# Kernel optimization log

Measured on AMD Instinct MI355X. Metric: run time of the kernel, lower is better.

## Reference

```python
import jax, jax.numpy as jnp
import numpy as np

N, IN_DIM, D, H, E_DIM, G, NPG = 512, 16, 256, 8, 6, 32, 16
C = D           # per-head channels in GATv2Conv/TransformerConv (out_channels=d_model)
HD = D // H     # MultiheadAttention head dim


def _ln(x, g, b, eps=1e-5):
    m = jnp.mean(x, -1, keepdims=True)
    v = jnp.mean((x - m) ** 2, -1, keepdims=True)
    return (x - m) * jax.lax.rsqrt(v + eps) * g + b


def _seg_softmax(logits, seg, n):
    # numerically stable softmax over edges grouped by destination node
    m = jax.ops.segment_max(logits, seg, num_segments=n)
    m = jnp.where(jnp.isfinite(m), m, 0.0)
    e = jnp.exp(logits - m[seg])
    s = jax.ops.segment_sum(e, seg, num_segments=n)
    return e / jnp.maximum(s[seg], 1e-16)


def _forward(x, edge_attr, emb_w, emb_b, emb_g, emb_bb, pe, gat_lw, gat_lb, gat_rw, gat_rb, gat_ew, gat_att, gat_bias, tq_w, tq_b, tk_w, tk_b, tv_w, tv_b, te_w, tskip_w, tskip_b, tbeta_w, ln_g, ln_b, mha_in_w, mha_in_b, mha_out_w, mha_out_b, pool_w, pool_b, c1_w, c1_b, c1_g, c1_bb, rb_w, rb_b, rb_g, rb_bb, c2_w, c2_b, edge_index, batch):
    src, dst = edge_index[0], edge_index[1]
    E = edge_attr.shape[0]
    # input embedding (Linear + LayerNorm) + learned positional encoding (eval: no dropout)
    h = _ln(x @ emb_w.T + emb_b, emb_g, emb_bb) + pe[:N]
    residual = h
    # --- GATv2Conv(d_model, d_model, heads=H, edge_dim=6, concat=False, add_self_loops=False) ---
    xl = (h @ gat_lw.T + gat_lb).reshape(N, H, C)          # source transform
    xr = (h @ gat_rw.T + gat_rb).reshape(N, H, C)          # target transform
    ee = (edge_attr @ gat_ew.T).reshape(E, H, C)
    z = jax.nn.leaky_relu(xl[src] + xr[dst] + ee, 0.2)
    a = _seg_softmax(jnp.einsum('ehc,hc->eh', z, gat_att), dst, N)
    x_gat = jax.ops.segment_sum(xl[src] * a[..., None], dst, num_segments=N).mean(1) + gat_bias
    x_gat = _ln(x_gat, ln_g, ln_b)
    # --- TransformerConv(d_model, d_model, heads=H, edge_dim=6, concat=False, beta=True) ---
    te = (edge_attr @ te_w.T).reshape(E, H, C)
    q = (x_gat @ tq_w.T + tq_b).reshape(N, H, C)[dst]
    k = (x_gat @ tk_w.T + tk_b).reshape(N, H, C)[src] + te
    v = (x_gat @ tv_w.T + tv_b).reshape(N, H, C)[src] + te
    a2 = _seg_softmax((q * k).sum(-1) / np.sqrt(C).astype(np.float32), dst, N)
    out = jax.ops.segment_sum(v * a2[..., None], dst, num_segments=N).mean(1)
    r = x_gat @ tskip_w.T + tskip_b
    beta = jax.nn.sigmoid(jnp.concatenate([out, r, out - r], -1) @ tbeta_w.T)
    x_tr = _ln(beta * r + (1.0 - beta) * out, ln_g, ln_b)
    # --- dynamic attention mask: after the repeat/permute/reshape gymnastics this equals
    #     ds[:N] repeated H*N times, reshaped to [H, N, N] ---
    im = edge_attr[:, 5]
    ds = jnp.exp(-0.5 * ((im - 125.09) / 15.0) ** 2)
    ds = 1.0 - (ds - ds.min()) / (ds.max() - ds.min())
    mask = jnp.repeat(ds[:N], H * N).reshape(H, N, N)
    # --- cross MultiheadAttention (query=x_tr, key=x_gat, value=h, attn_mask added) ---
    wq, wk, wv = jnp.split(mha_in_w, 3, axis=0)
    bq, bk, bv = jnp.split(mha_in_b, 3, axis=0)
    qh = ((x_tr @ wq.T + bq) / np.sqrt(HD).astype(np.float32)).reshape(N, H, HD).transpose(1, 0, 2)
    kh = (x_gat @ wk.T + bk).reshape(N, H, HD).transpose(1, 0, 2)
    vh = (h @ wv.T + bv).reshape(N, H, HD).transpose(1, 0, 2)
    attn = jax.nn.softmax(qh @ kh.transpose(0, 2, 1) + mask, axis=-1)   # [H,N,N]
    o = (attn @ vh).transpose(1, 0, 2).reshape(N, D) @ mha_out_w.T + mha_out_b
    # torch broadcast of [N,1,D] attn output + [N,D] residual -> [N,N,D]
    x3 = o[:, None, :] + residual[None, :, :]
    # attention pooling: softmax over a size-1 dim yields all-ones scores (kept faithfully)
    x2 = x3.reshape(N * N, D)
    brep = jnp.tile(batch, N)
    score = jax.nn.softmax(x2 @ pool_w.T + pool_b, axis=1)
    pooled = jax.ops.segment_sum(score * x2, brep, num_segments=G)
    # classifier: Linear->LN->GELU->ResidualBlockv2->Linear (dropout off in eval)
    c = jax.nn.gelu(_ln(pooled @ c1_w.T + c1_b, c1_g, c1_bb), approximate=False)
    c = c + jax.nn.gelu(_ln(c @ rb_w.T + rb_b, rb_g, rb_bb), approximate=False)
    return c @ c2_w.T + c2_b   # [G, 1]


def setup_inputs():
    key = jax.random.key(0)
    ks = iter(jax.random.split(key, 64))
    f = lambda *sh: 0.02 * jax.random.normal(next(ks), sh, jnp.float32)
    # G fully-connected directed cliques of NPG nodes (no self loops) -> every node has in-edges
    i = np.arange(NPG)
    s, t = np.meshgrid(i, i, indexing='ij')
    msk = s != t
    s, t = s[msk], t[msk]
    off = (np.arange(G) * NPG)[:, None]
    edge_index = jnp.asarray(np.stack([(s[None] + off).reshape(-1), (t[None] + off).reshape(-1)]), jnp.int32)
    E = edge_index.shape[1]
    batch = jnp.asarray(np.repeat(np.arange(G), NPG), jnp.int32)
    x = jax.random.normal(next(ks), (N, IN_DIM), jnp.float32)
    edge_attr = jax.random.normal(next(ks), (E, E_DIM), jnp.float32)
    edge_attr = edge_attr.at[:, 5].set(edge_attr[:, 5] * 30.0 + 125.0)  # invariant-mass-like column
    HC = H * C
    return dict(
        x=x, edge_attr=edge_attr,
        emb_w=f(D, IN_DIM), emb_b=f(D), emb_g=jnp.ones(D), emb_bb=jnp.zeros(D),
        pe=f(1000, D),
        gat_lw=f(HC, D), gat_lb=f(HC), gat_rw=f(HC, D), gat_rb=f(HC),
        gat_ew=f(HC, E_DIM), gat_att=f(H, C), gat_bias=f(C),
        tq_w=f(HC, D), tq_b=f(HC), tk_w=f(HC, D), tk_b=f(HC),
        tv_w=f(HC, D), tv_b=f(HC), te_w=f(HC, E_DIM),
        tskip_w=f(D, D), tskip_b=f(D), tbeta_w=f(1, 3 * D),
        ln_g=jnp.ones(D), ln_b=jnp.zeros(D),
        mha_in_w=f(3 * D, D), mha_in_b=f(3 * D), mha_out_w=f(D, D), mha_out_b=f(D),
        pool_w=f(1, D), pool_b=f(1),
        c1_w=f(128, D), c1_b=f(128), c1_g=jnp.ones(128), c1_bb=jnp.zeros(128),
        rb_w=f(128, 128), rb_b=f(128), rb_g=jnp.ones(128), rb_bb=jnp.zeros(128),
        c2_w=f(1, 128), c2_b=f(1),
        edge_index=edge_index, batch=batch)


def reference(x, edge_attr, emb_w, emb_b, emb_g, emb_bb, pe, gat_lw, gat_lb, gat_rw, gat_rb, gat_ew, gat_att, gat_bias, tq_w, tq_b, tk_w, tk_b, tv_w, tv_b, te_w, tskip_w, tskip_b, tbeta_w, ln_g, ln_b, mha_in_w, mha_in_b, mha_out_w, mha_out_b, pool_w, pool_b, c1_w, c1_b, c1_g, c1_bb, rb_w, rb_b, rb_g, rb_bb, c2_w, c2_b, edge_index, batch):
    return _forward(x, edge_attr, emb_w, emb_b, emb_g, emb_bb, pe, gat_lw, gat_lb, gat_rw, gat_rb, gat_ew, gat_att, gat_bias, tq_w, tq_b, tk_w, tk_b, tv_w, tv_b, te_w, tskip_w, tskip_b, tbeta_w, ln_g, ln_b, mha_in_w, mha_in_b, mha_out_w, mha_out_b, pool_w, pool_b, c1_w, c1_b, c1_g, c1_bb, rb_w, rb_b, rb_g, rb_bb, c2_w, c2_b, edge_index, batch)
```

## Files before the change

kernel.cpp:

```cpp
#include <hip/hip_runtime.h>
#include <hip/hip_bf16.h>
#include <math.h>

#define NN 512
#define DM 256
#define NH 8
#define NG 32
#define NPG 16
#define INDIM 16
#define BIGW (2048 * 256)

typedef __hip_bfloat16 bf16;
typedef __attribute__((ext_vector_type(8))) short short8;
typedef __attribute__((ext_vector_type(4))) float f32x4;

__device__ __forceinline__ float b2f(bf16 v) { return __bfloat162float(v); }
__device__ __forceinline__ bf16 f2b(float v) { return __float2bfloat16(v); }
__device__ __forceinline__ short f2bs(float v) { bf16 t = __float2bfloat16(v); return *(short*)&t; }
__device__ __forceinline__ float fin(float v) {
    return (v == v && v > -1e30f && v < 1e30f) ? v : 0.f;
}
__device__ __forceinline__ int is_bf16(const void* ones_arr) {
    return ((const unsigned short*)ones_arr)[0] == 0x3F80u;
}

__device__ __forceinline__ void unpack8(uint4 u, float* w) {
    unsigned uu[4] = {u.x, u.y, u.z, u.w};
    #pragma unroll
    for (int j = 0; j < 4; j++) {
        __hip_bfloat162 b2 = *reinterpret_cast<const __hip_bfloat162*>(&uu[j]);
        float2 f = __bfloat1622float2(b2);
        w[2 * j] = f.x; w[2 * j + 1] = f.y;
    }
}
__device__ __forceinline__ float4 bload4(const bf16* p) {
    uint2 u = *(const uint2*)p;
    __hip_bfloat162 a = *reinterpret_cast<const __hip_bfloat162*>(&u.x);
    __hip_bfloat162 b = *reinterpret_cast<const __hip_bfloat162*>(&u.y);
    float2 f0 = __bfloat1622float2(a), f1 = __bfloat1622float2(b);
    return make_float4(f0.x, f0.y, f1.x, f1.y);
}

__device__ __forceinline__ float dot256(const float* xrow, const bf16* wrow) {
    const uint4* w4 = (const uint4*)wrow;
    uint4 q = w4[0];
    float acc = 0.f;
    for (int k8 = 0; k8 < 32; k8++) {
        uint4 qn = w4[(k8 + 1) & 31];
        float w[8]; unpack8(q, w);
        const float4* sp = (const float4*)&xrow[k8 * 8];
        float4 a0 = sp[0], a1 = sp[1];
        acc += a0.x*w[0] + a0.y*w[1] + a0.z*w[2] + a0.w*w[3]
             + a1.x*w[4] + a1.y*w[5] + a1.z*w[6] + a1.w*w[7];
        q = qn;
    }
    return acc;
}

template<int BS>
__device__ __forceinline__ float ln_norm(float v, float g, float b, float* red) {
    int t = threadIdx.x;
    red[t] = v; __syncthreads();
    for (int s = BS / 2; s > 0; s >>= 1) { if (t < s) red[t] += red[t + s]; __syncthreads(); }
    float mean = red[0] * (1.0f / (float)BS); __syncthreads();
    float d = v - mean;
    red[t] = d * d; __syncthreads();
    for (int s = BS / 2; s > 0; s >>= 1) { if (t < s) red[t] += red[t + s]; __syncthreads(); }
    float var = red[0] * (1.0f / (float)BS); __syncthreads();
    return d * rsqrtf(var + 1e-5f) * g + b;
}

struct CvtTab { const void* p[35]; int cum[36]; };
struct Cvt5 { const void* p[5]; };
__global__ void k_convert_all(Cvt5 tab5, CvtTab tab, const void* ones, bf16* wbig,
                              bf16* wbuf, float* gz, int nz) {
    int i = blockIdx.x * 256 + threadIdx.x;
    int a = blockIdx.y;
    int bf = is_bf16(ones);
    if (a < 5) {
        if (i >= BIGW) return;
        float v = bf ? b2f(((const bf16*)tab5.p[a])[i]) : ((const float*)tab5.p[a])[i];
        int row = i >> 8, k = i & 255;
        int hh = row >> 8, col = row & 255;
        int T = col >> 4, n16 = col & 15;
        int ks = k >> 5, quad = (k >> 3) & 3, j = k & 7;
        int dst = ((((hh * 16 + T) * 8 + ks) * 4 + quad) * 16 + n16) * 8 + j;
        wbig[(size_t)a * BIGW + dst] = f2b(v);
    } else {
        if (i < tab.cum[35]) {
            int aa = 0;
            while (i >= tab.cum[aa + 1]) aa++;
            int off = i - tab.cum[aa];
            float v = bf ? b2f(((const bf16*)tab.p[aa])[off]) : ((const float*)tab.p[aa])[off];
            wbuf[i] = f2b(v);
        } else if (i < tab.cum[35] + nz) {
            gz[i - tab.cum[35]] = 0.f;
        }
    }
}

__global__ void k_embed(const bf16* xw, const bf16* emw, const bf16* emb, const bf16* emg,
                        const bf16* embb, const bf16* pe, float* h,
                        float* pre1, float* pre2, float* gsum_h) {
    int n = blockIdx.x, t = threadIdx.x;
    size_t gi = (size_t)n * DM + t;
    pre1[gi] = 0.f;
    pre2[gi] = 0.f;
    __shared__ float xin[INDIM];
    __shared__ float red[DM];
    if (t < INDIM) xin[t] = b2f(xw[n * INDIM + t]);
    __syncthreads();
    float acc = b2f(emb[t]);
    #pragma unroll
    for (int k = 0; k < INDIM; k++) acc += xin[k] * b2f(emw[t * INDIM + k]);
    float y = ln_norm<DM>(acc, b2f(emg[t]), b2f(embb[t]), red);
    float hv = fin(y + b2f(pe[gi]));
    h[gi] = hv;
    atomicAdd(&gsum_h[(n >> 4) * DM + t], hv);
}

__device__ __forceinline__ void row_softmax16(float* M, int tid) {
    if (tid < NPG) {
        float* row = M + tid * NPG;
        float m = -1e30f;
        #pragma unroll
        for (int s = 0; s < NPG; s++) m = fmaxf(m, row[s]);
        if (m < -1e29f) {
            #pragma unroll
            for (int s = 0; s < NPG; s++) row[s] = 0.f;
        } else {
            float sum = 0.f;
            #pragma unroll
            for (int s = 0; s < NPG; s++) sum += expf(row[s] - m);
            float inv = 1.f / fmaxf(sum, 1e-16f);
            #pragma unroll
            for (int s = 0; s < NPG; s++) row[s] = expf(row[s] - m) * inv;
        }
    }
}

__global__ __launch_bounds__(512, 1)
void k_gat_fused(const float* h, const bf16* lw, const bf16* rw,
                 const bf16* lb, const bf16* rbv, const bf16* eww, const bf16* attw,
                 const bf16* ea, const int* src, const int* dst, int epg, float* pre) {
    extern __shared__ char smraw[];
    int g = blockIdx.x, hh = blockIdx.y, tid = threadIdx.x;
    bf16* hb     = (bf16*)smraw;
    bf16* ew_s   = hb + NPG * DM;
    bf16* att_s  = ew_s + 6 * DM;
    float* ea_s  = (float*)(att_s + DM);
    float* Mx    = ea_s + 6 * epg;
    int* sl_s    = (int*)(Mx + NPG * NPG);
    int* dl_s    = sl_s + epg;
    bf16* xl_s   = (bf16*)(dl_s + epg);
    bf16* xr_s   = xl_s + NPG * DM;

    int ebase = g * epg;
    for (int i = tid; i < NPG * DM; i += 512) hb[i] = f2b(h[(size_t)g * NPG * DM + i]);
    for (int i = tid; i < 6 * DM; i += 512) {
        int f = i >> 8, cc = i & 255;
        ew_s[f * DM + cc] = eww[(size_t)(hh * DM + cc) * 6 + f];
    }
    if (tid < DM) att_s[tid] = attw[hh * DM + tid];
    for (int i = tid; i < 6 * epg; i += 512) {
        int f = i / epg, e = i - f * epg;
        ea_s[f * epg + e] = b2f(ea[(size_t)(ebase + e) * 6 + f]);
    }
    if (tid < NPG * NPG) Mx[tid] = -1e30f;
    if (tid < epg) {
        int e = ebase + tid;
        sl_s[tid] = (src[e] - g * NPG) & (NPG - 1);
        dl_s[tid] = (dst[e] - g * NPG) & (NPG - 1);
    }
    __syncthreads();

    int lane = tid & 63, wave = tid >> 6;
    int n16 = lane & 15, quad = lane >> 4;
    f32x4 accA[2], accB[2];
    #pragma unroll
    for (int ct = 0; ct < 2; ct++) { accA[ct] = (f32x4)0.f; accB[ct] = (f32x4)0.f; }
    for (int ks = 0; ks < 8; ks++) {
        short8 a8 = *(const short8*)&hb[n16 * DM + ks * 32 + quad * 8];
        #pragma unroll
        for (int ct = 0; ct < 2; ct++) {
            int T = ct * 8 + wave;
            size_t fo = (((size_t)(hh * 16 + T) * 8 + ks) * 4 + quad) * 128 + n16 * 8;
            short8 bL = *(const short8*)(lw + fo);
            short8 bR = *(const short8*)(rw + fo);
            accA[ct] = __builtin_amdgcn_mfma_f32_16x16x32_bf16(a8, bL, accA[ct], 0, 0, 0);
            accB[ct] = __builtin_amdgcn_mfma_f32_16x16x32_bf16(a8, bR, accB[ct], 0, 0, 0);
        }
    }
    #pragma unroll
    for (int ct = 0; ct < 2; ct++) {
        int col = (ct * 8 + wave) * 16 + n16;
        float blv = b2f(lb[hh * DM + col]), brv = b2f(rbv[hh * DM + col]);
        #pragma unroll
        for (int reg = 0; reg < 4; reg++) {
            int row = quad * 4 + reg;
            xl_s[row * DM + col] = f2b(accA[ct][reg] + blv);
            xr_s[row * DM + col] = f2b(accB[ct][reg] + brv);
        }
    }
    __syncthreads();

    int c4 = lane * 4;
    for (int ei = wave; ei < epg; ei += 8) {
        int sl = sl_s[ei], dl = dl_s[ei];
        float ee0 = 0.f, ee1 = 0.f, ee2 = 0.f, ee3 = 0.f;
        #pragma unroll
        for (int f = 0; f < 6; f++) {
            float eb = ea_s[f * epg + ei];
            float4 wf = bload4(&ew_s[f * DM + c4]);
            ee0 += eb * wf.x; ee1 += eb * wf.y; ee2 += eb * wf.z; ee3 += eb * wf.w;
        }
        float4 av = bload4(&att_s[c4]);
        float4 xlv = bload4(&xl_s[sl * DM + c4]);
        float4 xrv = bload4(&xr_s[dl * DM + c4]);
        float z0 = xlv.x + xrv.x + ee0;
        float z1 = xlv.y + xrv.y + ee1;
        float z2 = xlv.z + xrv.z + ee2;
        float z3 = xlv.w + xrv.w + ee3;
        z0 = (z0 >= 0.f) ? z0 : 0.2f * z0;
        z1 = (z1 >= 0.f) ? z1 : 0.2f * z1;
        z2 = (z2 >= 0.f) ? z2 : 0.2f * z2;
        z3 = (z3 >= 0.f) ? z3 : 0.2f * z3;
        float acc = z0 * av.x + z1 * av.y + z2 * av.z + z3 * av.w;
        #pragma unroll
        for (int off = 32; off > 0; off >>= 1) acc += __shfl_down(acc, off);
        if (lane == 0) Mx[dl * NPG + sl] = fin(acc);
    }
    __syncthreads();
    row_softmax16(Mx, tid);
    __syncthreads();

    int c = tid & 255, halfd = tid >> 8;
    float xlv[NPG];
    #pragma unroll
    for (int s = 0; s < NPG; s++) xlv[s] = b2f(xl_s[s * DM + c]);
    #pragma unroll
    for (int dd = 0; dd < 8; dd++) {
        int d = halfd * 8 + dd;
        const float* Ar = Mx + d * NPG;
        float acc = 0.f;
        #pragma unroll
        for (int s = 0; s < NPG; s++) acc += Ar[s] * xlv[s];
        atomicAdd(&pre[(size_t)(g * NPG + d) * DM + c], fin(acc));
    }
}

__global__ void k_gat_post_skip(const float* pre, const bf16* gat_bias, const bf16* lng,
                                const bf16* lnb, const bf16* skw, const bf16* skb,
                                float* x_gat, float* rbuf) {
    int n = blockIdx.x, t = threadIdx.x;
    __shared__ float red[DM];
    __shared__ float xrow[DM];
    float v = pre[(size_t)n * DM + t] * 0.125f + b2f(gat_bias[t]);
    float y = fin(ln_norm<DM>(v, b2f(lng[t]), b2f(lnb[t]), red));
    x_gat[(size_t)n * DM + t] = y;
    xrow[t] = y;
    __syncthreads();
    rbuf[(size_t)n * DM + t] = fin(dot256(xrow, skw + (size_t)t * DM) + b2f(skb[t]));
}

__global__ __launch_bounds__(512, 1)
void k_tr_fused(const float* xg, const bf16* qw, const bf16* kw, const bf16* vw,
                const bf16* qb, const bf16* kb, const bf16* vb, const bf16* tew,
                const bf16* ea, const int* src, const int* dst, int epg, float* pre) {
    extern __shared__ char smraw[];
    int g = blockIdx.x, hh = blockIdx.y, tid = threadIdx.x;
    bf16* hb    = (bf16*)smraw;
    bf16* tw_s  = hb + NPG * DM;
    float* ea_s = (float*)(tw_s + 6 * DM);
    float* Lqk  = ea_s + 6 * epg;
    float* Mx   = Lqk + NPG * NPG;
    float* P    = Mx + NPG * NPG;
    float* W6   = P + NPG * 6;
    int* emap   = (int*)(W6 + NPG * 6);
    int* sl_s   = emap + NPG * NPG;
    int* dl_s   = sl_s + epg;
    bf16* q_s   = (bf16*)(dl_s + epg);
    bf16* k_s   = q_s + NPG * DM;
    bf16* v_s   = k_s + NPG * DM;

    int ebase = g * epg;
    for (int i = tid; i < NPG * DM; i += 512) hb[i] = f2b(xg[(size_t)g * NPG * DM + i]);
    for (int i = tid; i < 6 * DM; i += 512) {
        int f = i >> 8, cc = i & 255;
        tw_s[f * DM + cc] = tew[(size_t)(hh * DM + cc) * 6 + f];
    }
    for (int i = tid; i < 6 * epg; i += 512) {
        int f = i / epg, e = i - f * epg;
        ea_s[f * epg + e] = b2f(ea[(size_t)(ebase + e) * 6 + f]);
    }
    if (tid < NPG * NPG) { Mx[tid] = -1e30f; emap[tid] = -1; }
    if (tid < epg) {
        int e = ebase + tid;
        sl_s[tid] = (src[e] - g * NPG) & (NPG - 1);
        dl_s[tid] = (dst[e] - g * NPG) & (NPG - 1);
    }
    __syncthreads();

    int lane = tid & 63, wave = tid >> 6;
    int n16 = lane & 15, quad = lane >> 4;
    f32x4 aQ[2], aK[2], aV[2];
    #pragma unroll
    for (int ct = 0; ct < 2; ct++) { aQ[ct] = (f32x4)0.f; aK[ct] = (f32x4)0.f; aV[ct] = (f32x4)0.f; }
    for (int ks = 0; ks < 8; ks++) {
        short8 a8 = *(const short8*)&hb[n16 * DM + ks * 32 + quad * 8];
        #pragma unroll
        for (int ct = 0; ct < 2; ct++) {
            int T = ct * 8 + wave;
            size_t fo = (((size_t)(hh * 16 + T) * 8 + ks) * 4 + quad) * 128 + n16 * 8;
            short8 bQ = *(const short8*)(qw + fo);
            short8 bK = *(const short8*)(kw + fo);
            short8 bV = *(const short8*)(vw + fo);
            aQ[ct] = __builtin_amdgcn_mfma_f32_16x16x32_bf16(a8, bQ, aQ[ct], 0, 0, 0);
            aK[ct] = __builtin_amdgcn_mfma_f32_16x16x32_bf16(a8, bK, aK[ct], 0, 0, 0);
            aV[ct] = __builtin_amdgcn_mfma_f32_16x16x32_bf16(a8, bV, aV[ct], 0, 0, 0);
        }
    }
    #pragma unroll
    for (int ct = 0; ct < 2; ct++) {
        int col = (ct * 8 + wave) * 16 + n16;
        float bq = b2f(qb[hh * DM + col]), bk = b2f(kb[hh * DM + col]), bv = b2f(vb[hh * DM + col]);
        #pragma unroll
        for (int reg = 0; reg < 4; reg++) {
            int row = quad * 4 + reg;
            q_s[row * DM + col] = f2b(aQ[ct][reg] + bq);
            k_s[row * DM + col] = f2b(aK[ct][reg] + bk);
            v_s[row * DM + col] = f2b(aV[ct][reg] + bv);
        }
    }
    __syncthreads();

    if (wave == 0) {
        f32x4 acc = (f32x4)0.f;
        for (int ks = 0; ks < 8; ks++) {
            short8 a8 = *(const short8*)&q_s[n16 * DM + ks * 32 + quad * 8];
            short8 b8 = *(const short8*)&k_s[n16 * DM + ks * 32 + quad * 8];
            acc = __builtin_amdgcn_mfma_f32_16x16x32_bf16(a8, b8, acc, 0, 0, 0);
        }
        #pragma unroll
        for (int reg = 0; reg < 4; reg++)
            Lqk[(quad * 4 + reg) * NPG + n16] = acc[reg];
    } else if (wave <= 2) {
        int idx = tid - 64;
        if (idx < NPG * 6) {
            int d = idx / 6, f = idx - d * 6;
            const bf16* qr = q_s + d * DM;
            const bf16* twr = tw_s + f * DM;
            float acc = 0.f;
            for (int cc = 0; cc < DM; cc += 4) {
                float4 qv = bload4(qr + cc);
                float4 t4 = bload4(twr + cc);
                acc += qv.x * t4.x + qv.y * t4.y + qv.z * t4.z + qv.w * t4.w;
            }
            P[idx] = acc;
        }
    }
    __syncthreads();

    if (tid < epg) {
        int sl = sl_s[tid], dl = dl_s[tid];
        float acc = Lqk[dl * NPG + sl];
        #pragma unroll
        for (int f = 0; f < 6; f++) acc += ea_s[f * epg + tid] * P[dl * 6 + f];
        Mx[dl * NPG + sl] = fin(acc * 0.0625f);
        emap[dl * NPG + sl] = tid;
    }
    __syncthreads();
    row_softmax16(Mx, tid);
    __syncthreads();
    if (tid < NPG * 6) {
        int d = tid / 6, f = tid - d * 6;
        float acc = 0.f;
        #pragma unroll
        for (int s = 0; s < NPG; s++) {
            int e = emap[d * NPG + s];
            if (e >= 0) acc += Mx[d * NPG + s] * ea_s[f * epg + e];
        }
        W6[tid] = acc;
    }
    __syncthreads();

    int c = tid & 255, halfd = tid >> 8;
    float vv[NPG];
    #pragma unroll
    for (int s = 0; s < NPG; s++) vv[s] = b2f(v_s[s * DM + c]);
    float twc[6];
    #pragma unroll
    for (int f = 0; f < 6; f++) twc[f] = b2f(tw_s[f * DM + c]);
    #pragma unroll
    for (int dd = 0; dd < 8; dd++) {
        int d = halfd * 8 + dd;
        const float* Ar = Mx + d * NPG;
        const float* Wr = W6 + d * 6;
        float acc = 0.f;
        #pragma unroll
        for (int s = 0; s < NPG; s++) acc += Ar[s] * vv[s];
        #pragma unroll
        for (int f = 0; f < 6; f++) acc += Wr[f] * twc[f];
        atomicAdd(&pre[(size_t)(g * NPG + d) * DM + c], fin(acc));
    }
}

__global__ void k_tr_post_qkv(const float* pre, const float* rbuf, const float* x_gat,
                              const float* h, const bf16* tbeta, const bf16* lng,
                              const bf16* lnb, const bf16* mw, const bf16* mb, float* qkv) {
    int n = blockIdx.x, t = threadIdx.x;
    __shared__ float red[DM];
    __shared__ float xtr_s[DM];
    __shared__ float xg_s[DM];
    __shared__ float h_s[DM];
    __shared__ float beta_sh;
    float outc = pre[(size_t)n * DM + t] * 0.125f;
    float rc = rbuf[(size_t)n * DM + t];
    xg_s[t] = x_gat[(size_t)n * DM + t];
    h_s[t] = h[(size_t)n * DM + t];
    float w1 = b2f(tbeta[t]), w2 = b2f(tbeta[DM + t]), w3 = b2f(tbeta[2 * DM + t]);
    red[t] = outc * (w1 + w3) + rc * (w2 - w3);
    __syncthreads();
    for (int s2 = 128; s2 > 0; s2 >>= 1) { if (t < s2) red[t] += red[t + s2]; __syncthreads(); }
    if (t == 0) beta_sh = 1.0f / (1.0f + expf(-red[0]));
    __syncthreads();
    float beta = beta_sh;
    float mix = beta * rc + (1.0f - beta) * outc;
    float y = fin(ln_norm<DM>(mix, b2f(lng[t]), b2f(lnb[t]), red));
    xtr_s[t] = y;
    __syncthreads();
    float q = (dot256(xtr_s, mw + (size_t)t * DM) + b2f(mb[t])) * 0.17677669529663689f;
    float k = dot256(xg_s, mw + (size_t)(DM + t) * DM) + b2f(mb[DM + t]);
    float v = dot256(h_s, mw + (size_t)(2 * DM + t) * DM) + b2f(mb[2 * DM + t]);
    qkv[(size_t)n * DM + t] = fin(q);
    qkv[((size_t)NN + n) * DM + t] = fin(k);
    qkv[((size_t)2 * NN + n) * DM + t] = fin(v);
}

#define SPAD 516
__global__ __launch_bounds__(256, 1)
void k_attn(const float* qh, const float* kh, const float* vh, float* ao) {
    extern __shared__ char sm[];
    bf16* KF   = (bf16*)sm;
    float* Sc  = (float*)(KF + 8192);
    float* Op  = Sc + 16 * SPAD;
    float* red = Op + 4 * 16 * 32;
    int qt = blockIdx.x, hd = blockIdx.y, tid = threadIdx.x;
    int lane = tid & 63, wave = tid >> 6, n16 = lane & 15, quad = lane >> 4;

    short8 a8q;
    {
        const float* qp = &qh[(size_t)(qt * 16 + n16) * DM + hd * 32 + quad * 8];
        float4 q0 = *(const float4*)qp, q1 = *((const float4*)qp + 1);
        a8q[0] = f2bs(q0.x); a8q[1] = f2bs(q0.y); a8q[2] = f2bs(q0.z); a8q[3] = f2bs(q0.w);
        a8q[4] = f2bs(q1.x); a8q[5] = f2bs(q1.y); a8q[6] = f2bs(q1.z); a8q[7] = f2bs(q1.w);
    }

    for (int half = 0; half < 2; half++) {
        __syncthreads();
        for (int i = tid; i < 8192; i += 256) {
            int jj = i >> 5, d = i & 31;
            bf16 val = f2b(kh[(size_t)(half * 256 + jj) * DM + hd * 32 + d]);
            int ktl = jj >> 4, nn = jj & 15, qd = d >> 3, j8 = d & 7;
            KF[((ktl * 4 + qd) * 16 + nn) * 8 + j8] = val;
        }
        __syncthreads();
        #pragma unroll
        for (int it = 0; it < 4; it++) {
            int ktl = wave * 4 + it;
            short8 b8 = *(const short8*)&KF[((ktl * 4 + quad) * 16 + n16) * 8];
            f32x4 acc = (f32x4)0.f;
            acc = __builtin_amdgcn_mfma_f32_16x16x32_bf16(a8q, b8, acc, 0, 0, 0);
            #pragma unroll
            for (int reg = 0; reg < 4; reg++)
                Sc[(quad * 4 + reg) * SPAD + half * 256 + ktl * 16 + n16] = acc[reg];
        }
    }
    __syncthreads();

    int r = tid >> 4, li = tid & 15;
    float m = -1e30f;
    for (int s = 0; s < 32; s++) m = fmaxf(m, Sc[r * SPAD + li + 16 * s]);
    red[r * 16 + li] = m; __syncthreads();
    for (int st = 8; st > 0; st >>= 1) {
        if (li < st) red[r * 16 + li] = fmaxf(red[r * 16 + li], red[r * 16 + li + st]);
        __syncthreads();
    }
    m = red[r * 16];
    __syncthreads();
    float sum = 0.f;
    for (int s = 0; s < 32; s++) sum += expf(Sc[r * SPAD + li + 16 * s] - m);
    red[r * 16 + li] = sum; __syncthreads();
    for (int st = 8; st > 0; st >>= 1) {
        if (li < st) red[r * 16 + li] += red[r * 16 + li + st];
        __syncthreads();
    }
    float inv = 1.0f / fmaxf(red[r * 16], 1e-16f);
    for (int s = 0; s < 32; s++) {
        int idx = r * SPAD + li + 16 * s;
        Sc[idx] = expf(Sc[idx] - m) * inv;
    }

    f32x4 o0 = (f32x4)0.f, o1 = (f32x4)0.f;
    for (int half = 0; half < 2; half++) {
        __syncthreads();
        for (int i = tid; i < 8192; i += 256) {
            int jj = i >> 5, d = i & 31;
            bf16 val = f2b(vh[(size_t)(half * 256 + jj) * DM + hd * 32 + d]);
            int ksl = jj >> 5, kin = jj & 31, qd = kin >> 3, j8 = kin & 7;
            int nn = d & 15, which = d >> 4;
            KF[which * 4096 + ((ksl * 4 + qd) * 16 + nn) * 8 + j8] = val;
        }
        __syncthreads();
        #pragma unroll
        for (int it = 0; it < 2; it++) {
            int ksl = wave * 2 + it;
            int ks = half * 8 + ksl;
            const float* sp = &Sc[n16 * SPAD + ks * 32 + quad * 8];
            float4 s0 = *(const float4*)sp, s1 = *((const float4*)sp + 1);
            short8 a8;
            a8[0] = f2bs(s0.x); a8[1] = f2bs(s0.y); a8[2] = f2bs(s0.z); a8[3] = f2bs(s0.w);
            a8[4] = f2bs(s1.x); a8[5] = f2bs(s1.y); a8[6] = f2bs(s1.z); a8[7] = f2bs(s1.w);
            short8 bv0 = *(const short8*)&KF[((ksl * 4 + quad) * 16 + n16) * 8];
            short8 bv1 = *(const short8*)&KF[4096 + ((ksl * 4 + quad) * 16 + n16) * 8];
            o0 = __builtin_amdgcn_mfma_f32_16x16x32_bf16(a8, bv0, o0, 0, 0, 0);
            o1 = __builtin_amdgcn_mfma_f32_16x16x32_bf16(a8, bv1, o1, 0, 0, 0);
        }
    }
    #pragma unroll
    for (int reg = 0; reg < 4; reg++) {
        Op[wave * 512 + (quad * 4 + reg) * 32 + n16] = o0[reg];
        Op[wave * 512 + (quad * 4 + reg) * 32 + 16 + n16] = o1[reg];
    }
    __syncthreads();
    for (int e = tid; e < 512; e += 256) {
        float v = Op[e] + Op[512 + e] + Op[1024 + e] + Op[1536 + e];
        ao[(size_t)(qt * 16 + (e >> 5)) * DM + hd * 32 + (e & 31)] = fin(v);
    }
}

__global__ void k_outproj(const float* ao, const bf16* W, const bf16* B,
                          float* obuf, float* gsum_o) {
    int n = blockIdx.x, t = threadIdx.x;
    __shared__ float xrow[DM];
    xrow[t] = ao[(size_t)n * DM + t];
    __syncthreads();
    float v = fin(dot256(xrow, W + (size_t)t * DM) + b2f(B[t]));
    obuf[(size_t)n * DM + t] = v;
    atomicAdd(&gsum_o[(n >> 4) * DM + t], v);
}

__global__ void k_mlp(const float* gsum_o, const float* gsum_h,
                      const bf16* c1_w, const bf16* c1_b, const bf16* c1_g,
                      const bf16* c1_bb, const bf16* rb_w, const bf16* rb_b,
                      const bf16* rb_g, const bf16* rb_bb, const bf16* c2_w,
                      const bf16* c2_b, const void* ones, void* out) {
    int g = blockIdx.x, t = threadIdx.x;
    __shared__ float pl[DM];
    __shared__ float u[128];
    __shared__ float red[128];
    float os0 = 0.f, os1 = 0.f;
    #pragma unroll
    for (int b = 0; b < NG; b++) {
        os0 += gsum_o[b * DM + t];
        os1 += gsum_o[b * DM + t + 128];
    }
    pl[t]       = fin((float)NPG * os0 + (float)NN * gsum_h[g * DM + t]);
    pl[t + 128] = fin((float)NPG * os1 + (float)NN * gsum_h[g * DM + t + 128]);
    __syncthreads();
    float acc = dot256(pl, c1_w + (size_t)t * DM) + b2f(c1_b[t]);
    float y = ln_norm<128>(acc, b2f(c1_g[t]), b2f(c1_bb[t]), red);
    float gl = 0.5f * y * (1.0f + erff(y * 0.70710678118654752f));
    u[t] = gl; __syncthreads();
    float acc2 = b2f(rb_b[t]);
    for (int k = 0; k < 128; k++) acc2 += u[k] * b2f(rb_w[(size_t)t * 128 + k]);
    float y2 = ln_norm<128>(acc2, b2f(rb_g[t]), b2f(rb_bb[t]), red);
    float cfin = gl + 0.5f * y2 * (1.0f + erff(y2 * 0.70710678118654752f));
    red[t] = cfin * b2f(c2_w[t]);
    __syncthreads();
    for (int s2 = 64; s2 > 0; s2 >>= 1) { if (t < s2) red[t] += red[t + s2]; __syncthreads(); }
    if (t == 0) {
        float res = fin(red[0] + b2f(c2_b[0]));
        if (is_bf16(ones)) ((bf16*)out)[g] = f2b(res);
        else               ((float*)out)[g] = res;
    }
}

extern "C" void kernel_launch(void* const* d_in, const int* in_sizes, int n_in,
                              void* d_out, int out_size, void* d_ws, size_t ws_size,
                              hipStream_t stream) {
    const int E = in_sizes[1] / 6;
    const int epg = E / NG;
    const int* eidx = (const int*)d_in[42];
    const int* srcp = eidx;
    const int* dstp = eidx + E;
    const void* ones = d_in[4];

    static const int idxs[35] = {0,1,2,3,4,5,6,8,10,11,12,13,15,17,19,20,21,22,23,24,
                                 25,26,27,28,29,32,33,34,35,36,37,38,39,40,41};
    CvtTab tab;
    int wOff[44];
    int cum = 0;
    for (int a = 0; a < 35; a++) {
        tab.p[a] = d_in[idxs[a]];
        tab.cum[a] = cum;
        wOff[idxs[a]] = cum;
        cum += in_sizes[idxs[a]];
    }
    tab.cum[35] = cum;
    const int totalW = cum;
    Cvt5 tab5;
    tab5.p[0] = d_in[7];  tab5.p[1] = d_in[9];
    tab5.p[2] = d_in[14]; tab5.p[3] = d_in[16]; tab5.p[4] = d_in[18];

    bf16* wbuf = (bf16*)d_ws;
    size_t wbytes = ((size_t)totalW * 2 + 255) & ~(size_t)255;
    float* fb = (float*)((char*)d_ws + wbytes);
    const size_t SL = (size_t)NN * DM;
    float* h      = fb;
    float* x_gat  = fb + SL;
    float* rbuf   = fb + 2 * SL;
    float* pre1   = fb + 3 * SL;
    float* pre2   = fb + 4 * SL;
    float* qkv    = fb + 5 * SL;
    float* gsum_o = fb + 8 * SL;
    float* gsum_h = gsum_o + NG * DM;
    bf16* wbig = (bf16*)qkv;
    float* ao = pre1;
    float* obuf = pre2;
    const int NZ = 2 * NG * DM;

    #define WB(i) (wbuf + wOff[i])

    int gx_small = (totalW + NZ + 255) / 256;
    int gx = BIGW / 256;
    if (gx_small > gx) gx = gx_small;
    k_convert_all<<<dim3(gx, 6), 256, 0, stream>>>(tab5, tab, ones, wbig, wbuf, gsum_o, NZ);

    k_embed<<<NN, DM, 0, stream>>>(WB(0), WB(2), WB(3), WB(4), WB(5), WB(6), h,
                                   pre1, pre2, gsum_h);

    int gat_lds = NPG*DM*2 + 6*DM*2 + DM*2 + (6*epg + NPG*NPG + 2*epg) * 4
                + 2*NPG*DM*2 + 16;
    k_gat_fused<<<dim3(NG, NH), 512, gat_lds, stream>>>(
        h, wbig, wbig + BIGW, WB(8), WB(10), WB(11), WB(12), WB(1), srcp, dstp, epg, pre1);
    k_gat_post_skip<<<NN, DM, 0, stream>>>(pre1, WB(13), WB(24), WB(25), WB(21), WB(22),
                                           x_gat, rbuf);

    int tr_lds = NPG*DM*2 + 6*DM*2 + (6*epg + 2*NPG*NPG + 2*NPG*6) * 4
               + (NPG*NPG + 2*epg) * 4 + 3*NPG*DM*2 + 16;
    k_tr_fused<<<dim3(NG, NH), 512, tr_lds, stream>>>(
        x_gat, wbig + 2 * (size_t)BIGW, wbig + 3 * (size_t)BIGW, wbig + 4 * (size_t)BIGW,
        WB(15), WB(17), WB(19), WB(20), WB(1), srcp, dstp, epg, pre2);
    k_tr_post_qkv<<<NN, DM, 0, stream>>>(pre2, rbuf, x_gat, h, WB(23), WB(24), WB(25),
                                         WB(26), WB(27), qkv);

    int attn_lds = 8192 * 2 + (16 * SPAD + 4 * 16 * 32 + 16 * 16) * 4;
    k_attn<<<dim3(NN / 16, NH), 256, attn_lds, stream>>>(qkv, qkv + SL, qkv + 2 * SL, ao);
    k_outproj<<<NN, DM, 0, stream>>>(ao, WB(28), WB(29), obuf, gsum_o);

    k_mlp<<<NG, 128, 0, stream>>>(gsum_o, gsum_h, WB(32), WB(33), WB(34), WB(35),
                                  WB(36), WB(37), WB(38), WB(39), WB(40), WB(41),
                                  ones, d_out);
    #undef WB
}
```

Before: 295.7 us.

## Transpose GEMV weights for coalesced reads and fold embedding into convert kernel

The weight-conversion kernel now also writes k-major, interleaved-by-4 copies of the skip, MHA in-projection and out-projection weights. The row-per-thread GEMVs in the skip, qkv and out-projection kernels use these copies, so neighbouring threads read neighbouring 8-byte chunks instead of each walking its own strided 512-byte row. The separate embedding launch is merged into the convert kernel as an extra grid slice, which saves one launch. The atomic per-graph sum of h is dropped and recomputed directly inside the MLP kernel. The cost is extra conversion work and transposed-weight storage in the workspace.

New measurement: 272.7 us. -7.8%, faster.

```diff
diff --git a/kernel.cpp b/kernel.cpp
--- a/kernel.cpp
+++ b/kernel.cpp
@@ -9,6 +9,10 @@
 #define NPG 16
 #define INDIM 16
 #define BIGW (2048 * 256)
+#define WT_SKIP 0
+#define WT_MHA  65536
+#define WT_OUT  (65536 + 196608)
+#define WT_TOTAL (65536 + 196608 + 65536)
 
 typedef __hip_bfloat16 bf16;
 typedef __attribute__((ext_vector_type(8))) short short8;
@@ -22,6 +26,9 @@
 }
 __device__ __forceinline__ int is_bf16(const void* ones_arr) {
     return ((const unsigned short*)ones_arr)[0] == 0x3F80u;
+}
+__device__ __forceinline__ float ldv(const void* p, size_t i, int bf) {
+    return bf ? b2f(((const bf16*)p)[i]) : ((const float*)p)[i];
 }
 
 __device__ __forceinline__ void unpack8(uint4 u, float* w) {
@@ -57,6 +64,20 @@
     return acc;
 }
 
+__device__ __forceinline__ float dot256T(const float* xrow, const bf16* wt, int r) {
+    float acc = 0.f;
+    #pragma unroll 8
+    for (int k4 = 0; k4 < 64; k4++) {
+        uint2 u = *(const uint2*)(wt + ((size_t)k4 * 256 + r) * 4);
+        __hip_bfloat162 b0 = *reinterpret_cast<const __hip_bfloat162*>(&u.x);
+        __hip_bfloat162 b1 = *reinterpret_cast<const __hip_bfloat162*>(&u.y);
+        float2 f0 = __bfloat1622float2(b0), f1 = __bfloat1622float2(b1);
+        float4 xv = *(const float4*)&xrow[k4 * 4];
+        acc += xv.x * f0.x + xv.y * f0.y + xv.z * f1.x + xv.w * f1.y;
+    }
+    return acc;
+}
+
 template<int BS>
 __device__ __forceinline__ float ln_norm(float v, float g, float b, float* red) {
     int t = threadIdx.x;
@@ -73,7 +94,8 @@
 struct CvtTab { const void* p[35]; int cum[36]; };
 struct Cvt5 { const void* p[5]; };
 __global__ void k_convert_all(Cvt5 tab5, CvtTab tab, const void* ones, bf16* wbig,
-                              bf16* wbuf, float* gz, int nz) {
+                              bf16* wbuf, float* gz, int nz, bf16* wt,
+                              float* pre1, float* pre2, float* h) {
     int i = blockIdx.x * 256 + threadIdx.x;
     int a = blockIdx.y;
     int bf = is_bf16(ones);
@@ -86,37 +108,49 @@
         int ks = k >> 5, quad = (k >> 3) & 3, j = k & 7;
         int dst = ((((hh * 16 + T) * 8 + ks) * 4 + quad) * 16 + n16) * 8 + j;
         wbig[(size_t)a * BIGW + dst] = f2b(v);
-    } else {
+    } else if (a == 5) {
         if (i < tab.cum[35]) {
             int aa = 0;
             while (i >= tab.cum[aa + 1]) aa++;
-            int off = i - tab.cum[aa];
-            float v = bf ? b2f(((const bf16*)tab.p[aa])[off]) : ((const float*)tab.p[aa])[off];
-            wbuf[i] = f2b(v);
+            wbuf[i] = f2b(ldv(tab.p[aa], i - tab.cum[aa], bf));
         } else if (i < tab.cum[35] + nz) {
             gz[i - tab.cum[35]] = 0.f;
-        }
-    }
-}
-
-__global__ void k_embed(const bf16* xw, const bf16* emw, const bf16* emb, const bf16* emg,
-                        const bf16* embb, const bf16* pe, float* h,
-                        float* pre1, float* pre2, float* gsum_h) {
-    int n = blockIdx.x, t = threadIdx.x;
-    size_t gi = (size_t)n * DM + t;
-    pre1[gi] = 0.f;
-    pre2[gi] = 0.f;
-    __shared__ float xin[INDIM];
-    __shared__ float red[DM];
-    if (t < INDIM) xin[t] = b2f(xw[n * INDIM + t]);
-    __syncthreads();
-    float acc = b2f(emb[t]);
-    #pragma unroll
-    for (int k = 0; k < INDIM; k++) acc += xin[k] * b2f(emw[t * INDIM + k]);
-    float y = ln_norm<DM>(acc, b2f(emg[t]), b2f(embb[t]), red);
-    float hv = fin(y + b2f(pe[gi]));
-    h[gi] = hv;
-    atomicAdd(&gsum_h[(n >> 4) * DM + t], hv);
+        } else if (i < tab.cum[35] + nz + WT_TOTAL) {
+            int off = i - tab.cum[35] - nz;
+            if (off < 65536) {
+                int row = off >> 8, k = off & 255;
+                wt[WT_SKIP + ((k >> 2) * 256 + row) * 4 + (k & 3)] =
+                    f2b(ldv(tab.p[16], off, bf));
+            } else if (off < 65536 + 196608) {
+                int o2 = off - 65536;
+                int row = o2 >> 8, k = o2 & 255;
+                int which = row >> 8, r = row & 255;
+                wt[WT_MHA + which * 65536 + ((k >> 2) * 256 + r) * 4 + (k & 3)] =
+                    f2b(ldv(tab.p[21], o2, bf));
+            } else {
+                int o2 = off - 65536 - 196608;
+                int row = o2 >> 8, k = o2 & 255;
+                wt[WT_OUT + ((k >> 2) * 256 + row) * 4 + (k & 3)] =
+                    f2b(ldv(tab.p[23], o2, bf));
+            }
+        }
+    } else {
+        int n = blockIdx.x;
+        if (n >= NN) return;
+        int t = threadIdx.x;
+        size_t gi = (size_t)n * DM + t;
+        pre1[gi] = 0.f;
+        pre2[gi] = 0.f;
+        __shared__ float xin[INDIM];
+        __shared__ float red[DM];
+        if (t < INDIM) xin[t] = ldv(tab.p[0], n * INDIM + t, bf);
+        __syncthreads();
+        float acc = ldv(tab.p[3], t, bf);
+        #pragma unroll
+        for (int k = 0; k < INDIM; k++) acc += xin[k] * ldv(tab.p[2], t * INDIM + k, bf);
+        float y = ln_norm<DM>(acc, ldv(tab.p[4], t, bf), ldv(tab.p[5], t, bf), red);
+        h[gi] = fin(y + ldv(tab.p[6], gi, bf));
+    }
 }
 
 __device__ __forceinline__ void row_softmax16(float* M, int tid) {
@@ -250,7 +284,7 @@
 }
 
 __global__ void k_gat_post_skip(const float* pre, const bf16* gat_bias, const bf16* lng,
-                                const bf16* lnb, const bf16* skw, const bf16* skb,
+                                const bf16* lnb, const bf16* wt, const bf16* skb,
                                 float* x_gat, float* rbuf) {
     int n = blockIdx.x, t = threadIdx.x;
     __shared__ float red[DM];
@@ -260,7 +294,7 @@
     x_gat[(size_t)n * DM + t] = y;
     xrow[t] = y;
     __syncthreads();
-    rbuf[(size_t)n * DM + t] = fin(dot256(xrow, skw + (size_t)t * DM) + b2f(skb[t]));
+    rbuf[(size_t)n * DM + t] = fin(dot256T(xrow, wt + WT_SKIP, t) + b2f(skb[t]));
 }
 
 __global__ __launch_bounds__(512, 1)
@@ -407,7 +441,7 @@
 
 __global__ void k_tr_post_qkv(const float* pre, const float* rbuf, const float* x_gat,
                               const float* h, const bf16* tbeta, const bf16* lng,
-                              const bf16* lnb, const bf16* mw, const bf16* mb, float* qkv) {
+                              const bf16* lnb, const bf16* wt, const bf16* mb, float* qkv) {
     int n = blockIdx.x, t = threadIdx.x;
     __shared__ float red[DM];
     __shared__ float xtr_s[DM];
@@ -429,9 +463,9 @@
     float y = fin(ln_norm<DM>(mix, b2f(lng[t]), b2f(lnb[t]), red));
     xtr_s[t] = y;
     __syncthreads();
-    float q = (dot256(xtr_s, mw + (size_t)t * DM) + b2f(mb[t])) * 0.17677669529663689f;
-    float k = dot256(xg_s, mw + (size_t)(DM + t) * DM) + b2f(mb[DM + t]);
-    float v = dot256(h_s, mw + (size_t)(2 * DM + t) * DM) + b2f(mb[2 * DM + t]);
+    float q = (dot256T(xtr_s, wt + WT_MHA, t) + b2f(mb[t])) * 0.17677669529663689f;
+    float k = dot256T(xg_s, wt + WT_MHA + 65536, t) + b2f(mb[DM + t]);
+    float v = dot256T(h_s, wt + WT_MHA + 131072, t) + b2f(mb[2 * DM + t]);
     qkv[(size_t)n * DM + t] = fin(q);
     qkv[((size_t)NN + n) * DM + t] = fin(k);
     qkv[((size_t)2 * NN + n) * DM + t] = fin(v);
@@ -539,18 +573,18 @@
     }
 }
 
-__global__ void k_outproj(const float* ao, const bf16* W, const bf16* B,
+__global__ void k_outproj(const float* ao, const bf16* wt, const bf16* B,
                           float* obuf, float* gsum_o) {
     int n = blockIdx.x, t = threadIdx.x;
     __shared__ float xrow[DM];
     xrow[t] = ao[(size_t)n * DM + t];
     __syncthreads();
-    float v = fin(dot256(xrow, W + (size_t)t * DM) + b2f(B[t]));
+    float v = fin(dot256T(xrow, wt + WT_OUT, t) + b2f(B[t]));
     obuf[(size_t)n * DM + t] = v;
     atomicAdd(&gsum_o[(n >> 4) * DM + t], v);
 }
 
-__global__ void k_mlp(const float* gsum_o, const float* gsum_h,
+__global__ void k_mlp(const float* gsum_o, const float* h,
                       const bf16* c1_w, const bf16* c1_b, const bf16* c1_g,
                       const bf16* c1_bb, const bf16* rb_w, const bf16* rb_b,
                       const bf16* rb_g, const bf16* rb_bb, const bf16* c2_w,
@@ -559,14 +593,19 @@
     __shared__ float pl[DM];
     __shared__ float u[128];
     __shared__ float red[128];
-    float os0 = 0.f, os1 = 0.f;
+    float os0 = 0.f, os1 = 0.f, hs0 = 0.f, hs1 = 0.f;
     #pragma unroll
     for (int b = 0; b < NG; b++) {
         os0 += gsum_o[b * DM + t];
         os1 += gsum_o[b * DM + t + 128];
     }
-    pl[t]       = fin((float)NPG * os0 + (float)NN * gsum_h[g * DM + t]);
-    pl[t + 128] = fin((float)NPG * os1 + (float)NN * gsum_h[g * DM + t + 128]);
+    #pragma unroll
+    for (int j = 0; j < NPG; j++) {
+        hs0 += h[(size_t)(g * NPG + j) * DM + t];
+        hs1 += h[(size_t)(g * NPG + j) * DM + t + 128];
+    }
+    pl[t]       = fin((float)NPG * os0 + (float)NN * hs0);
+    pl[t + 128] = fin((float)NPG * os1 + (float)NN * hs1);
     __syncthreads();
     float acc = dot256(pl, c1_w + (size_t)t * DM) + b2f(c1_b[t]);
     float y = ln_norm<128>(acc, b2f(c1_g[t]), b2f(c1_bb[t]), red);
@@ -624,27 +663,25 @@
     float* pre2   = fb + 4 * SL;
     float* qkv    = fb + 5 * SL;
     float* gsum_o = fb + 8 * SL;
-    float* gsum_h = gsum_o + NG * DM;
+    bf16* wt      = (bf16*)(gsum_o + NG * DM);
     bf16* wbig = (bf16*)qkv;
     float* ao = pre1;
     float* obuf = pre2;
-    const int NZ = 2 * NG * DM;
+    const int NZ = NG * DM;
 
     #define WB(i) (wbuf + wOff[i])
 
-    int gx_small = (totalW + NZ + 255) / 256;
+    int need5 = totalW + NZ + WT_TOTAL;
     int gx = BIGW / 256;
-    if (gx_small > gx) gx = gx_small;
-    k_convert_all<<<dim3(gx, 6), 256, 0, stream>>>(tab5, tab, ones, wbig, wbuf, gsum_o, NZ);
-
-    k_embed<<<NN, DM, 0, stream>>>(WB(0), WB(2), WB(3), WB(4), WB(5), WB(6), h,
-                                   pre1, pre2, gsum_h);
+    if ((need5 + 255) / 256 > gx) gx = (need5 + 255) / 256;
+    k_convert_all<<<dim3(gx, 7), 256, 0, stream>>>(tab5, tab, ones, wbig, wbuf,
+                                                   gsum_o, NZ, wt, pre1, pre2, h);
 
     int gat_lds = NPG*DM*2 + 6*DM*2 + DM*2 + (6*epg + NPG*NPG + 2*epg) * 4
                 + 2*NPG*DM*2 + 16;
     k_gat_fused<<<dim3(NG, NH), 512, gat_lds, stream>>>(
         h, wbig, wbig + BIGW, WB(8), WB(10), WB(11), WB(12), WB(1), srcp, dstp, epg, pre1);
-    k_gat_post_skip<<<NN, DM, 0, stream>>>(pre1, WB(13), WB(24), WB(25), WB(21), WB(22),
+    k_gat_post_skip<<<NN, DM, 0, stream>>>(pre1, WB(13), WB(24), WB(25), wt, WB(22),
                                            x_gat, rbuf);
 
     int tr_lds = NPG*DM*2 + 6*DM*2 + (6*epg + 2*NPG*NPG + 2*NPG*6) * 4
@@ -653,13 +690,13 @@
         x_gat, wbig + 2 * (size_t)BIGW, wbig + 3 * (size_t)BIGW, wbig + 4 * (size_t)BIGW,
         WB(15), WB(17), WB(19), WB(20), WB(1), srcp, dstp, epg, pre2);
     k_tr_post_qkv<<<NN, DM, 0, stream>>>(pre2, rbuf, x_gat, h, WB(23), WB(24), WB(25),
-                                         WB(26), WB(27), qkv);
+                                         wt, WB(27), qkv);
 
     int attn_lds = 8192 * 2 + (16 * SPAD + 4 * 16 * 32 + 16 * 16) * 4;
     k_attn<<<dim3(NN / 16, NH), 256, attn_lds, stream>>>(qkv, qkv + SL, qkv + 2 * SL, ao);
-    k_outproj<<<NN, DM, 0, stream>>>(ao, WB(28), WB(29), obuf, gsum_o);
-
-    k_mlp<<<NG, 128, 0, stream>>>(gsum_o, gsum_h, WB(32), WB(33), WB(34), WB(35),
+    k_outproj<<<NN, DM, 0, stream>>>(ao, wt, WB(29), obuf, gsum_o);
+
+    k_mlp<<<NG, 128, 0, stream>>>(gsum_o, h, WB(32), WB(33), WB(34), WB(35),
                                   WB(36), WB(37), WB(38), WB(39), WB(40), WB(41),
                                   ones, d_out);
     #undef WB
```
